# Optimization experiments

Measured on AMD Instinct MI355X. Metric: run time of the kernel, lower is better.

Reference implementation:

```python
import jax, jax.numpy as jnp
import numpy as np

B, N, C, DIN, DOUT = 16, 65536, 256, 16, 16  # ratio = N // C = 256 nodes per cluster


def setup_inputs() -> dict:
    key = jax.random.key(0)
    k1, k2, k3, k4, k5 = jax.random.split(key, 5)
    stdv = 1.0 / np.sqrt(DOUT)
    x = jax.random.normal(k1, (B, N, DIN), dtype=jnp.float32)
    # parameters, pre-reshaped: torch w_diag (in*out, C) with out-major io axis -> (out, in, C)
    w_diag = jax.random.uniform(k2, (DOUT, DIN, C), jnp.float32, -stdv, stdv)
    w_off = jax.random.uniform(k3, (DOUT, DIN, C, C), jnp.float32, -stdv, stdv)
    b1 = jax.random.uniform(k4, (DOUT,), jnp.float32, -stdv, stdv)
    # flatten_ids(cluster_ids): a permutation putting each cluster's nodes contiguous
    permute_ids = jax.random.permutation(k5, N)
    return {"x": x, "w_diag": w_diag, "w_off": w_off, "b1": b1, "permute_ids": permute_ids}


def reference(x, w_diag, w_off, b1, permute_ids):
    # Faithful to: W = rearrange(kron(diag_embed(w_diag), I_r)) + (1/N) rearrange(kron(w_off, 1_{rxr}))
    # out = inv_permute( reshape( W @ flatten(permute(x)) ) ) + b1,
    # computed via the block-constant structure instead of materializing the (Dout*N, Din*N) W.
    Bq, Nn, Din = x.shape
    Dout, _, Cc = w_diag.shape
    ratio = Nn // Cc
    inv_permute = jnp.argsort(permute_ids)
    xp = x[:, permute_ids, :]                       # (B, N, Din), cluster-contiguous
    xc = xp.reshape(Bq, Cc, ratio, Din)             # (B, C, r, Din)
    # diagonal blocks: per-cluster Din->Dout mixing, identity over within-cluster index
    out_diag = jnp.einsum('oic,bcri->bcro', w_diag, xc)   # (B, C, r, Dout)
    # off blocks: constant within each (cluster j, cluster k) block -> use cluster sums
    s = xc.sum(axis=2)                              # (B, C, Din)
    out_off = jnp.einsum('oick,bki->bco', w_off, s) / Nn  # (B, C, Dout)
    out = out_diag + out_off[:, :, None, :]         # broadcast over within-cluster index
    out = out.reshape(Bq, Nn, Dout)[:, inv_permute, :] + b1[None, None, :]
    return out
```

## Files before the change

### kernel.cpp

```cpp
#include <hip/hip_runtime.h>

#define B_    16
#define N_    65536
#define C_    256
#define DIN_  16
#define DOUT_ 16

typedef float f32x4 __attribute__((ext_vector_type(4)));


__global__ __launch_bounds__(256) void k_sum_prep(
    const float* __restrict__ x, const float* __restrict__ w_diag,
    const int* __restrict__ P, float* __restrict__ s,
    float* __restrict__ wd_t, int* __restrict__ c_of_n)
{
    int bid = blockIdx.x;
    int t = threadIdx.x;
    if (bid >= B_ * C_) {
        int r = bid - B_ * C_;
        if (r < 256) {
            int o = r >> 4, i = r & 15;
            wd_t[t * 256 + i * 16 + o] = w_diag[r * C_ + t];
        } else {
            int k = r - 256;
            c_of_n[P[k * 256 + t]] = k;
        }
        return;
    }
    int b = bid >> 8;
    int k = bid & (C_ - 1);
    int q  = t & 3;
    int rg = t >> 2;
    float4 acc = make_float4(0.f, 0.f, 0.f, 0.f);
    const int jbase = k << 8;
    #pragma unroll
    for (int m = 0; m < 4; ++m) {
        int n = P[jbase + rg + 64 * m];
        const float4* row =
            reinterpret_cast<const float4*>(x + ((size_t)(b * N_ + n)) * DIN_);
        float4 v = row[q];
        acc.x += v.x; acc.y += v.y; acc.z += v.z; acc.w += v.w;
    }
    #pragma unroll
    for (int mask = 4; mask <= 32; mask <<= 1) {
        acc.x += __shfl_xor(acc.x, mask, 64);
        acc.y += __shfl_xor(acc.y, mask, 64);
        acc.z += __shfl_xor(acc.z, mask, 64);
        acc.w += __shfl_xor(acc.w, mask, 64);
    }
    __shared__ float4 part[4][4];
    int lane = t & 63, wave = t >> 6;
    if (lane < 4) part[wave][lane] = acc;
    __syncthreads();
    if (t < 16) {
        int qq = t >> 2, comp = t & 3;
        float v = 0.f;
        #pragma unroll
        for (int w = 0; w < 4; ++w) {
            const float* p = reinterpret_cast<const float*>(&part[w][qq]);
            v += p[comp];
        }
        int i = qq * 4 + comp;
        s[(b * DIN_ + i) * C_ + k] = v;
    }
}

__global__ __launch_bounds__(512, 4) void k_off(
    const float* __restrict__ w_off, const float* __restrict__ s,
    const float* __restrict__ b1, float* __restrict__ off)
{
    const int g  = (int)blockIdx.x;
    const int c  = g & 255;
    const int b0 = (g >> 8) * 8;
    const int t  = threadIdx.x;
    const int kq = t & 63;
    const int wv = t >> 6;
    const int o0 = wv * 2;

    const float4* w4 = reinterpret_cast<const float4*>(w_off);
    const float4* s4 = reinterpret_cast<const float4*>(s);

    const int wb0 = ((o0 * 16) * 256 + c) * 64 + kq;
    const int wb1 = wb0 + 262144;
    const int sb  = (b0 * 16) * 64 + kq;

    float acc[16];
    #pragma unroll
    for (int z = 0; z < 16; ++z) acc[z] = 0.f;

    #pragma unroll
    for (int i = 0; i < DIN_; ++i) {
        float4 w0 = w4[wb0 + i * 16384];
        float4 w1 = w4[wb1 + i * 16384];
        #pragma unroll
        for (int bb = 0; bb < 8; ++bb) {
            float4 sv = s4[sb + (bb * 16 + i) * 64];
            acc[bb]     += w0.x * sv.x + w0.y * sv.y + w0.z * sv.z + w0.w * sv.w;
            acc[8 + bb] += w1.x * sv.x + w1.y * sv.y + w1.z * sv.z + w1.w * sv.w;
        }
    }

#define FOLD(MASK, CNT)                                                        \
    {                                                                          \
        const bool hi_ = (kq & (MASK)) != 0;                                   \
        _Pragma("unroll")                                                      \
        for (int j = 0; j < (CNT); ++j) {                                      \
            float keep = hi_ ? acc[j + (CNT)] : acc[j];                        \
            float send = hi_ ? acc[j] : acc[j + (CNT)];                        \
            acc[j] = keep + __shfl_xor(send, (MASK), 64);                      \
        }                                                                      \
    }
    FOLD(1, 8) FOLD(2, 4) FOLD(4, 2) FOLD(8, 1)
#undef FOLD
    acc[0] += __shfl_xor(acc[0], 16, 64);
    acc[0] += __shfl_xor(acc[0], 32, 64);

    if (kq < 16) {
        int j  = ((kq & 1) << 3) | ((kq & 2) << 1) | ((kq & 4) >> 1) | ((kq & 8) >> 3);
        int oo = j >> 3;
        int bb = j & 7;
        int b  = b0 + bb;
        int o  = o0 + oo;
        off[((b << 8) + c) * DOUT_ + o] = acc[0] * (1.0f / (float)N_) + b1[o];
    }
}

__global__ __launch_bounds__(256) void k_apply_seq(
    const float* __restrict__ x, const int* __restrict__ c_of_n,
    const float* __restrict__ wd_t, const float* __restrict__ off,
    float* __restrict__ out)
{
    int t = threadIdx.x;
    int lr = t >> 2, q = t & 3;
    int n = blockIdx.x * 64 + lr;
    int c = c_of_n[n];

    const float4* wd4 = reinterpret_cast<const float4*>(wd_t);
    float4 wds[16];
    #pragma unroll
    for (int i = 0; i < 16; ++i) wds[i] = wd4[c * 64 + i * 4 + q];

    const float4* x4   = reinterpret_cast<const float4*>(x);
    const float4* off4 = reinterpret_cast<const float4*>(off);
    f32x4* out4        = reinterpret_cast<f32x4*>(out);

    #pragma unroll 2
    for (int b = 0; b < B_; ++b) {
        size_t rowbase = ((size_t)(b * N_ + n)) * 4;
        float4 x0 = x4[rowbase + 0];
        float4 x1 = x4[rowbase + 1];
        float4 x2 = x4[rowbase + 2];
        float4 x3 = x4[rowbase + 3];
        float4 acc = off4[((size_t)((b << 8) + c)) * 4 + q];
        float xv[16];
        xv[0]=x0.x; xv[1]=x0.y; xv[2]=x0.z; xv[3]=x0.w;
        xv[4]=x1.x; xv[5]=x1.y; xv[6]=x1.z; xv[7]=x1.w;
        xv[8]=x2.x; xv[9]=x2.y; xv[10]=x2.z; xv[11]=x2.w;
        xv[12]=x3.x; xv[13]=x3.y; xv[14]=x3.z; xv[15]=x3.w;
        #pragma unroll
        for (int i = 0; i < 16; ++i) {
            acc.x += xv[i] * wds[i].x;
            acc.y += xv[i] * wds[i].y;
            acc.z += xv[i] * wds[i].z;
            acc.w += xv[i] * wds[i].w;
        }
        f32x4 accv;
        accv.x = acc.x; accv.y = acc.y; accv.z = acc.z; accv.w = acc.w;
        __builtin_nontemporal_store(accv, &out4[rowbase + q]);
    }
}

extern "C" void kernel_launch(void* const* d_in, const int* in_sizes, int n_in,
                              void* d_out, int out_size, void* d_ws, size_t ws_size,
                              hipStream_t stream) {
    const float* x      = (const float*)d_in[0];
    const float* w_diag = (const float*)d_in[1];
    const float* w_off  = (const float*)d_in[2];
    const float* b1     = (const float*)d_in[3];
    const int*   P      = (const int*)d_in[4];
    float* out    = (float*)d_out;
    float* s      = (float*)d_ws;
    float* off    = s + 65536;
    float* wd_t   = off + 65536;
    int*   c_of_n = (int*)(wd_t + 65536);

    k_sum_prep<<<B_ * C_ + 512, 256, 0, stream>>>(x, w_diag, P, s, wd_t, c_of_n);
    k_off<<<512, 512, 0, stream>>>(w_off, s, b1, off);
    k_apply_seq<<<N_ / 64, 256, 0, stream>>>(x, c_of_n, wd_t, off, out);
}
```

Measured before the change: 214.5 us.

## Split k_off over input-channel chunks with atomic accumulation for more parallelism

k_off now runs 4096 blocks of 256 threads instead of 512 blocks of 512. Each block handles 4 outputs, 4 inputs and 4 batches per wave. Partial sums over the input-channel split are combined with atomicAdd into an off buffer that the prep kernel pre-fills with the bias. All weight and cluster-sum loads are issued up front behind a sched barrier, to raise memory-level parallelism on the 64 MB w_off stream. This adds atomic traffic and makes the float summation order nondeterministic.

```diff
diff --git a/kernel.cpp b/kernel.cpp
--- a/kernel.cpp
+++ b/kernel.cpp
@@ -11,8 +11,9 @@
 
 __global__ __launch_bounds__(256) void k_sum_prep(
     const float* __restrict__ x, const float* __restrict__ w_diag,
-    const int* __restrict__ P, float* __restrict__ s,
-    float* __restrict__ wd_t, int* __restrict__ c_of_n)
+    const int* __restrict__ P, const float* __restrict__ b1,
+    float* __restrict__ s, float* __restrict__ wd_t,
+    int* __restrict__ c_of_n, float* __restrict__ off)
 {
     int bid = blockIdx.x;
     int t = threadIdx.x;
@@ -21,9 +22,12 @@
         if (r < 256) {
             int o = r >> 4, i = r & 15;
             wd_t[t * 256 + i * 16 + o] = w_diag[r * C_ + t];
-        } else {
+        } else if (r < 512) {
             int k = r - 256;
             c_of_n[P[k * 256 + t]] = k;
+        } else {
+            int m = (r - 512) * 256 + t;
+            off[m] = b1[m & 15];
         }
         return;
     }
@@ -65,38 +69,50 @@
     }
 }
 
-__global__ __launch_bounds__(512, 4) void k_off(
+__global__ __launch_bounds__(256) void k_off(
     const float* __restrict__ w_off, const float* __restrict__ s,
-    const float* __restrict__ b1, float* __restrict__ off)
+    float* __restrict__ off)
 {
     const int g  = (int)blockIdx.x;
     const int c  = g & 255;
-    const int b0 = (g >> 8) * 8;
+    const int o0 = ((g >> 8) & 3) * 4;
+    const int i0 = (g >> 10) * 4;
     const int t  = threadIdx.x;
     const int kq = t & 63;
-    const int wv = t >> 6;
-    const int o0 = wv * 2;
+    const int b0 = (t >> 6) * 4;
 
     const float4* w4 = reinterpret_cast<const float4*>(w_off);
     const float4* s4 = reinterpret_cast<const float4*>(s);
 
-    const int wb0 = ((o0 * 16) * 256 + c) * 64 + kq;
-    const int wb1 = wb0 + 262144;
-    const int sb  = (b0 * 16) * 64 + kq;
+    float4 wv[4][4];
+    float4 sv[4][4];
+    #pragma unroll
+    for (int ii = 0; ii < 4; ++ii) {
+        const int i = i0 + ii;
+        #pragma unroll
+        for (int oo = 0; oo < 4; ++oo)
+            wv[ii][oo] = w4[(((o0 + oo) * 16 + i) * 256 + c) * 64 + kq];
+        #pragma unroll
+        for (int bb = 0; bb < 4; ++bb)
+            sv[ii][bb] = s4[((b0 + bb) * 16 + i) * 64 + kq];
+    }
+    __builtin_amdgcn_sched_barrier(0);
 
     float acc[16];
     #pragma unroll
     for (int z = 0; z < 16; ++z) acc[z] = 0.f;
 
     #pragma unroll
-    for (int i = 0; i < DIN_; ++i) {
-        float4 w0 = w4[wb0 + i * 16384];
-        float4 w1 = w4[wb1 + i * 16384];
-        #pragma unroll
-        for (int bb = 0; bb < 8; ++bb) {
-            float4 sv = s4[sb + (bb * 16 + i) * 64];
-            acc[bb]     += w0.x * sv.x + w0.y * sv.y + w0.z * sv.z + w0.w * sv.w;
-            acc[8 + bb] += w1.x * sv.x + w1.y * sv.y + w1.z * sv.z + w1.w * sv.w;
+    for (int ii = 0; ii < 4; ++ii) {
+        #pragma unroll
+        for (int oo = 0; oo < 4; ++oo) {
+            #pragma unroll
+            for (int bb = 0; bb < 4; ++bb) {
+                acc[oo * 4 + bb] += wv[ii][oo].x * sv[ii][bb].x
+                                  + wv[ii][oo].y * sv[ii][bb].y
+                                  + wv[ii][oo].z * sv[ii][bb].z
+                                  + wv[ii][oo].w * sv[ii][bb].w;
+            }
         }
     }
 
@@ -117,11 +133,11 @@
 
     if (kq < 16) {
         int j  = ((kq & 1) << 3) | ((kq & 2) << 1) | ((kq & 4) >> 1) | ((kq & 8) >> 3);
-        int oo = j >> 3;
-        int bb = j & 7;
+        int oo = j >> 2;
+        int bb = j & 3;
         int b  = b0 + bb;
         int o  = o0 + oo;
-        off[((b << 8) + c) * DOUT_ + o] = acc[0] * (1.0f / (float)N_) + b1[o];
+        atomicAdd(&off[((b << 8) + c) * DOUT_ + o], acc[0] * (1.0f / (float)N_));
     }
 }
 
@@ -184,7 +200,8 @@
     float* wd_t   = off + 65536;
     int*   c_of_n = (int*)(wd_t + 65536);
 
-    k_sum_prep<<<B_ * C_ + 512, 256, 0, stream>>>(x, w_diag, P, s, wd_t, c_of_n);
-    k_off<<<512, 512, 0, stream>>>(w_off, s, b1, off);
+    k_sum_prep<<<B_ * C_ + 768, 256, 0, stream>>>(x, w_diag, P, b1,
+                                                  s, wd_t, c_of_n, off);
+    k_off<<<4096, 256, 0, stream>>>(w_off, s, off);
     k_apply_seq<<<N_ / 64, 256, 0, stream>>>(x, c_of_n, wd_t, off, out);
 }
```

Result: faster. 197.3 us (-8.0%).
